# Kernel optimization log

Hardware: AMD Instinct MI355X
Metric: run time of the kernel (lower is better)

Reference implementation:

```python
import jax, jax.numpy as jnp
import numpy as np

N_EDGES = 1_600_000
D_FEAT = 32
N_NODES = 50_000


def setup_inputs() -> dict:
    key = jax.random.key(0)
    k1, k2, k3, k4 = jax.random.split(key, 4)
    m = jax.random.normal(k1, (N_EDGES, D_FEAT), dtype=jnp.float32)
    dst = jax.random.randint(k2, (N_EDGES,), 0, N_NODES, dtype=jnp.int64)
    w = jax.random.normal(k3, (4,), dtype=jnp.float32)
    b = jax.random.normal(k4, (1,), dtype=jnp.float32)
    return {"m": m, "dst": dst, "w": w, "b": b, "n_nodes": N_NODES}


def reference(m, dst, w, b, n_nodes):
    # Four segment reductions edge->node over destination index (copy_e_*)
    s = jax.ops.segment_sum(m, dst, num_segments=n_nodes)            # [N, D]
    mn = jax.ops.segment_min(m, dst, num_segments=n_nodes)
    mx = jax.ops.segment_max(m, dst, num_segments=n_nodes)
    deg = jax.ops.segment_sum(jnp.ones((m.shape[0],), m.dtype), dst,
                              num_segments=n_nodes)                  # [N]
    has = (deg > 0)[:, None]
    # DGL returns 0 for zero-degree nodes
    mn = jnp.where(has, mn, 0.0)
    mx = jnp.where(has, mx, 0.0)
    mean = s / jnp.maximum(deg, 1.0)[:, None]
    stacked = jnp.stack([s, mn, mx, mean], axis=-1)                  # [N, D, 4]
    out = jnp.einsum('ndk,k->nd', stacked, w) + b[0]                 # Dense(4,1) + squeeze
    return out
```

## Files before the change

kernel.cpp:

```cpp
#include <hip/hip_runtime.h>
#include <math.h>

#define D_FEAT 32
#define BSHIFT 5
#define NODES_PER_BKT 32
#define TILE 8192
#define PT 32
#define MAXBKT 2048
#define CAP 2048

__global__ void hist_kernel(const int* __restrict__ dst, int* __restrict__ bucketCount,
                            int E4, int nbucket) {
    __shared__ int h[MAXBKT];
    for (int i = threadIdx.x; i < nbucket; i += 256) h[i] = 0;
    __syncthreads();
    const int4* dst4 = (const int4*)dst;
    int tbase4 = blockIdx.x * (TILE / 4);
    #pragma unroll
    for (int k = 0; k < PT / 4; k++) {
        int i4 = tbase4 + k * 256 + threadIdx.x;
        if (i4 < E4) {
            int4 d = dst4[i4];
            atomicAdd(&h[d.x >> BSHIFT], 1);
            atomicAdd(&h[d.y >> BSHIFT], 1);
            atomicAdd(&h[d.z >> BSHIFT], 1);
            atomicAdd(&h[d.w >> BSHIFT], 1);
        }
    }
    __syncthreads();
    for (int i = threadIdx.x; i < nbucket; i += 256) {
        int c = h[i];
        if (c) atomicAdd(&bucketCount[i], c);
    }
}

__global__ void scan_kernel(const int* __restrict__ bucketCount,
                            int* __restrict__ bucketBase, int* __restrict__ bucketCursor,
                            int nbucket, int E) {
    __shared__ int lds[256];
    int tid = threadIdx.x;
    int vals[8];
    int s = 0;
    #pragma unroll
    for (int k = 0; k < 8; k++) {
        int i = tid * 8 + k;
        vals[k] = (i < nbucket) ? bucketCount[i] : 0;
        s += vals[k];
    }
    lds[tid] = s;
    __syncthreads();
    for (int off = 1; off < 256; off <<= 1) {
        int t = (tid >= off) ? lds[tid - off] : 0;
        __syncthreads();
        lds[tid] += t;
        __syncthreads();
    }
    int run = lds[tid] - s;
    #pragma unroll
    for (int k = 0; k < 8; k++) {
        int i = tid * 8 + k;
        if (i < nbucket) { bucketBase[i] = run; bucketCursor[i] = run; }
        run += vals[k];
    }
    if (tid == 0) bucketBase[nbucket] = E;
}

__global__ void partition_kernel(const int* __restrict__ dst,
                                 int* __restrict__ bucketCursor,
                                 unsigned int* __restrict__ keys,
                                 int E4, int nbucket) {
    __shared__ int h[MAXBKT];
    __shared__ int baseL[MAXBKT];
    int tid = threadIdx.x;
    for (int i = tid; i < nbucket; i += 256) h[i] = 0;
    __syncthreads();
    const int4* dst4 = (const int4*)dst;
    int tbase4 = blockIdx.x * (TILE / 4);
    int pk[PT];
    #pragma unroll
    for (int k = 0; k < PT / 4; k++) {
        int i4 = tbase4 + k * 256 + tid;
        if (i4 < E4) {
            int4 d = dst4[i4];
            int b0 = d.x >> BSHIFT; int r0 = atomicAdd(&h[b0], 1);
            int b1 = d.y >> BSHIFT; int r1 = atomicAdd(&h[b1], 1);
            int b2 = d.z >> BSHIFT; int r2 = atomicAdd(&h[b2], 1);
            int b3 = d.w >> BSHIFT; int r3 = atomicAdd(&h[b3], 1);
            pk[4 * k + 0] = (b0 << 18) | ((d.x & (NODES_PER_BKT - 1)) << 13) | r0;
            pk[4 * k + 1] = (b1 << 18) | ((d.y & (NODES_PER_BKT - 1)) << 13) | r1;
            pk[4 * k + 2] = (b2 << 18) | ((d.z & (NODES_PER_BKT - 1)) << 13) | r2;
            pk[4 * k + 3] = (b3 << 18) | ((d.w & (NODES_PER_BKT - 1)) << 13) | r3;
        } else {
            pk[4 * k + 0] = -1; pk[4 * k + 1] = -1;
            pk[4 * k + 2] = -1; pk[4 * k + 3] = -1;
        }
    }
    __syncthreads();
    for (int i = tid; i < nbucket; i += 256) {
        int c = h[i];
        baseL[i] = c ? atomicAdd(&bucketCursor[i], c) : 0;
    }
    __syncthreads();
    #pragma unroll
    for (int k = 0; k < PT / 4; k++) {
        int i4 = tbase4 + k * 256 + tid;
        int e = i4 * 4;
        #pragma unroll
        for (int l = 0; l < 4; l++) {
            int p = pk[4 * k + l];
            if (p >= 0) {
                int b   = p >> 18;
                int loc = (p >> 13) & (NODES_PER_BKT - 1);
                int r   = p & 8191;
                keys[baseL[b] + r] = ((unsigned)loc << 26) | (unsigned)(e + l);
            }
        }
    }
}

__global__ __launch_bounds__(256) void bucket_gather_kernel(
        const float* __restrict__ m,
        const unsigned int* __restrict__ keys,
        const int* __restrict__ bucketBase,
        const float* __restrict__ w,
        const float* __restrict__ bia,
        float* __restrict__ out, int N) {
    __shared__ unsigned int ukey[CAP];
    __shared__ int seid[CAP];
    __shared__ int nh[NODES_PER_BKT];
    __shared__ int noff[NODES_PER_BKT + 1];
    __shared__ int ncur[NODES_PER_BKT];
    int bkt = blockIdx.x;
    int tid = threadIdx.x;
    int start = bucketBase[bkt];
    int cnt = bucketBase[bkt + 1] - start;
    if (cnt > CAP) cnt = CAP;

    if (tid < NODES_PER_BKT) nh[tid] = 0;
    __syncthreads();
    for (int i = tid; i < cnt; i += 256) {
        unsigned int k = keys[start + i];
        ukey[i] = k;
        atomicAdd(&nh[k >> 26], 1);
    }
    __syncthreads();
    if (tid < NODES_PER_BKT) {
        int v = nh[tid];
        int x = v;
        #pragma unroll
        for (int off = 1; off < NODES_PER_BKT; off <<= 1) {
            int t = __shfl_up(x, off, 64);
            if (tid >= off) x += t;
        }
        noff[tid + 1] = x;
        if (tid == 0) noff[0] = 0;
        ncur[tid] = x - v;
    }
    __syncthreads();
    for (int i = tid; i < cnt; i += 256) {
        unsigned int k = ukey[i];
        int pos = atomicAdd(&ncur[k >> 26], 1);
        seid[pos] = (int)(k & 0x03FFFFFFu);
    }
    __syncthreads();

    const int fo  = tid & 7;
    const int grp = tid >> 3;
    const int node = (bkt << BSHIFT) + grp;
    const int s0 = noff[grp];
    const int e0 = noff[grp + 1];
    const int deg = e0 - s0;
    const float w0 = w[0], w1 = w[1], w2 = w[2], w3 = w[3], bb = bia[0];

    float sa0 = 0.f, sa1 = 0.f, sa2 = 0.f, sa3 = 0.f;
    float mn0 = INFINITY, mn1 = INFINITY, mn2 = INFINITY, mn3 = INFINITY;
    float mx0 = -INFINITY, mx1 = -INFINITY, mx2 = -INFINITY, mx3 = -INFINITY;

#define ACC(v)                                              \
    sa0 += (v).x; mn0 = fminf(mn0, (v).x); mx0 = fmaxf(mx0, (v).x); \
    sa1 += (v).y; mn1 = fminf(mn1, (v).y); mx1 = fmaxf(mx1, (v).y); \
    sa2 += (v).z; mn2 = fminf(mn2, (v).z); mx2 = fmaxf(mx2, (v).z); \
    sa3 += (v).w; mn3 = fminf(mn3, (v).w); mx3 = fmaxf(mx3, (v).w);

    int j = s0;
    for (; j + 4 <= e0; j += 4) {
        int ea = seid[j], eb = seid[j + 1], ec = seid[j + 2], ed = seid[j + 3];
        float4 va = *(const float4*)&m[ea * D_FEAT + (fo << 2)];
        float4 vb = *(const float4*)&m[eb * D_FEAT + (fo << 2)];
        float4 vc = *(const float4*)&m[ec * D_FEAT + (fo << 2)];
        float4 vd = *(const float4*)&m[ed * D_FEAT + (fo << 2)];
        ACC(va); ACC(vb); ACC(vc); ACC(vd);
    }
    for (; j < e0; j++) {
        float4 v = *(const float4*)&m[seid[j] * D_FEAT + (fo << 2)];
        ACC(v);
    }
#undef ACC

    if (node < N) {
        bool has = deg > 0;
        float inv = 1.0f / fmaxf((float)deg, 1.0f);
        float4 o;
        o.x = w0 * sa0 + w1 * (has ? mn0 : 0.f) + w2 * (has ? mx0 : 0.f) + w3 * (sa0 * inv) + bb;
        o.y = w0 * sa1 + w1 * (has ? mn1 : 0.f) + w2 * (has ? mx1 : 0.f) + w3 * (sa1 * inv) + bb;
        o.z = w0 * sa2 + w1 * (has ? mn2 : 0.f) + w2 * (has ? mx2 : 0.f) + w3 * (sa2 * inv) + bb;
        o.w = w0 * sa3 + w1 * (has ? mn3 : 0.f) + w2 * (has ? mx3 : 0.f) + w3 * (sa3 * inv) + bb;
        *(float4*)&out[node * D_FEAT + (fo << 2)] = o;
    }
}

extern "C" void kernel_launch(void* const* d_in, const int* in_sizes, int n_in,
                              void* d_out, int out_size, void* d_ws, size_t ws_size,
                              hipStream_t stream) {
    const float* m   = (const float*)d_in[0];
    const int*   dst = (const int*)  d_in[1];
    const float* w   = (const float*)d_in[2];
    const float* b   = (const float*)d_in[3];

    int E = in_sizes[0] / D_FEAT;
    int N = out_size    / D_FEAT;
    int E4 = E / 4;
    int nbucket = (N + NODES_PER_BKT - 1) >> BSHIFT;

    int* ws           = (int*)d_ws;
    int* bucketCount  = ws;
    int* bucketBase   = bucketCount + MAXBKT;
    int* bucketCursor = bucketBase + MAXBKT + 1;
    unsigned int* keys = (unsigned int*)(bucketCursor + MAXBKT);

    int nTiles = (E + TILE - 1) / TILE;

    hipMemsetAsync(bucketCount, 0, MAXBKT * sizeof(int), stream);
    hipLaunchKernelGGL(hist_kernel, dim3(nTiles), dim3(256), 0, stream,
                       dst, bucketCount, E4, nbucket);
    hipLaunchKernelGGL(scan_kernel, dim3(1), dim3(256), 0, stream,
                       bucketCount, bucketBase, bucketCursor, nbucket, E);
    hipLaunchKernelGGL(partition_kernel, dim3(nTiles), dim3(256), 0, stream,
                       dst, bucketCursor, keys, E4, nbucket);
    hipLaunchKernelGGL(bucket_gather_kernel, dim3(nbucket), dim3(256), 0, stream,
                       m, keys, bucketBase, w, b, (float*)d_out, N);
}
```

Measured before the change: 335.1 us.

## Widen buckets to 128 nodes and stage partitioned keys in LDS

Buckets grow from 32 to 128 nodes, so there are 391 buckets instead of 1563. The partition kernel now does a local scan and stages keys in shared memory sorted by bucket, then writes each bucket's run to global memory, instead of scattering keys directly. The gather kernel uses 512 threads that loop over two node groups, with a larger seid buffer and no ukey copy, re-reading keys from global memory. The goal is fewer global atomics on the bucket cursors and more contiguous key writes, at the cost of a large LDS footprint (32 KB stage buffer) and a copy loop where each thread serially writes one bucket's run.

```diff
diff --git a/kernel.cpp b/kernel.cpp
--- a/kernel.cpp
+++ b/kernel.cpp
@@ -2,17 +2,19 @@
 #include <math.h>
 
 #define D_FEAT 32
-#define BSHIFT 5
-#define NODES_PER_BKT 32
+#define BSHIFT 7
+#define NODES_PER_BKT 128
 #define TILE 8192
 #define PT 32
-#define MAXBKT 2048
-#define CAP 2048
-
-__global__ void hist_kernel(const int* __restrict__ dst, int* __restrict__ bucketCount,
-                            int E4, int nbucket) {
+#define MAXBKT 512
+#define CAPG 5120
+#define GBLK 512
+
+__global__ __launch_bounds__(256) void hist_kernel(const int* __restrict__ dst,
+                                                   int* __restrict__ bucketCount,
+                                                   int E4, int nbucket) {
     __shared__ int h[MAXBKT];
-    for (int i = threadIdx.x; i < nbucket; i += 256) h[i] = 0;
+    for (int i = threadIdx.x; i < MAXBKT; i += 256) h[i] = 0;
     __syncthreads();
     const int4* dst4 = (const int4*)dst;
     int tbase4 = blockIdx.x * (TILE / 4);
@@ -34,19 +36,15 @@
     }
 }
 
-__global__ void scan_kernel(const int* __restrict__ bucketCount,
-                            int* __restrict__ bucketBase, int* __restrict__ bucketCursor,
-                            int nbucket, int E) {
+__global__ __launch_bounds__(256) void scan_kernel(const int* __restrict__ bucketCount,
+                                                   int* __restrict__ bucketBase,
+                                                   int* __restrict__ bucketCursor,
+                                                   int nbucket, int E) {
     __shared__ int lds[256];
     int tid = threadIdx.x;
-    int vals[8];
-    int s = 0;
-    #pragma unroll
-    for (int k = 0; k < 8; k++) {
-        int i = tid * 8 + k;
-        vals[k] = (i < nbucket) ? bucketCount[i] : 0;
-        s += vals[k];
-    }
+    int v0 = bucketCount[2 * tid];
+    int v1 = bucketCount[2 * tid + 1];
+    int s = v0 + v1;
     lds[tid] = s;
     __syncthreads();
     for (int off = 1; off < 256; off <<= 1) {
@@ -56,77 +54,91 @@
         __syncthreads();
     }
     int run = lds[tid] - s;
-    #pragma unroll
-    for (int k = 0; k < 8; k++) {
-        int i = tid * 8 + k;
-        if (i < nbucket) { bucketBase[i] = run; bucketCursor[i] = run; }
-        run += vals[k];
-    }
-    if (tid == 0) bucketBase[nbucket] = E;
-}
-
-__global__ void partition_kernel(const int* __restrict__ dst,
-                                 int* __restrict__ bucketCursor,
-                                 unsigned int* __restrict__ keys,
-                                 int E4, int nbucket) {
+    bucketBase[2 * tid] = run;       bucketCursor[2 * tid] = run;
+    bucketBase[2 * tid + 1] = run + v0; bucketCursor[2 * tid + 1] = run + v0;
+    if (tid == 255) bucketBase[512] = run + s;
+}
+
+__global__ __launch_bounds__(256) void partition_kernel(const int* __restrict__ dst,
+                                                        int* __restrict__ bucketCursor,
+                                                        unsigned int* __restrict__ keys,
+                                                        int E4, int nbucket) {
     __shared__ int h[MAXBKT];
-    __shared__ int baseL[MAXBKT];
+    __shared__ int hoff[MAXBKT + 1];
+    __shared__ int gbase[MAXBKT];
+    __shared__ int scanb[256];
+    __shared__ unsigned int stage[TILE];
     int tid = threadIdx.x;
-    for (int i = tid; i < nbucket; i += 256) h[i] = 0;
+    for (int i = tid; i < MAXBKT; i += 256) h[i] = 0;
     __syncthreads();
     const int4* dst4 = (const int4*)dst;
     int tbase4 = blockIdx.x * (TILE / 4);
-    int pk[PT];
     #pragma unroll
     for (int k = 0; k < PT / 4; k++) {
         int i4 = tbase4 + k * 256 + tid;
         if (i4 < E4) {
             int4 d = dst4[i4];
-            int b0 = d.x >> BSHIFT; int r0 = atomicAdd(&h[b0], 1);
-            int b1 = d.y >> BSHIFT; int r1 = atomicAdd(&h[b1], 1);
-            int b2 = d.z >> BSHIFT; int r2 = atomicAdd(&h[b2], 1);
-            int b3 = d.w >> BSHIFT; int r3 = atomicAdd(&h[b3], 1);
-            pk[4 * k + 0] = (b0 << 18) | ((d.x & (NODES_PER_BKT - 1)) << 13) | r0;
-            pk[4 * k + 1] = (b1 << 18) | ((d.y & (NODES_PER_BKT - 1)) << 13) | r1;
-            pk[4 * k + 2] = (b2 << 18) | ((d.z & (NODES_PER_BKT - 1)) << 13) | r2;
-            pk[4 * k + 3] = (b3 << 18) | ((d.w & (NODES_PER_BKT - 1)) << 13) | r3;
-        } else {
-            pk[4 * k + 0] = -1; pk[4 * k + 1] = -1;
-            pk[4 * k + 2] = -1; pk[4 * k + 3] = -1;
-        }
-    }
-    __syncthreads();
+            atomicAdd(&h[d.x >> BSHIFT], 1);
+            atomicAdd(&h[d.y >> BSHIFT], 1);
+            atomicAdd(&h[d.z >> BSHIFT], 1);
+            atomicAdd(&h[d.w >> BSHIFT], 1);
+        }
+    }
+    __syncthreads();
+    int v0 = h[2 * tid], v1 = h[2 * tid + 1];
+    int s = v0 + v1;
+    scanb[tid] = s;
+    __syncthreads();
+    for (int off = 1; off < 256; off <<= 1) {
+        int t = (tid >= off) ? scanb[tid - off] : 0;
+        __syncthreads();
+        scanb[tid] += t;
+        __syncthreads();
+    }
+    int run = scanb[tid] - s;
+    hoff[2 * tid] = run;
+    hoff[2 * tid + 1] = run + v0;
+    if (tid == 255) hoff[512] = run + s;
     for (int i = tid; i < nbucket; i += 256) {
         int c = h[i];
-        baseL[i] = c ? atomicAdd(&bucketCursor[i], c) : 0;
-    }
+        gbase[i] = c ? atomicAdd(&bucketCursor[i], c) : 0;
+    }
+    __syncthreads();
+    for (int i = tid; i < MAXBKT; i += 256) h[i] = hoff[i];
     __syncthreads();
     #pragma unroll
     for (int k = 0; k < PT / 4; k++) {
         int i4 = tbase4 + k * 256 + tid;
-        int e = i4 * 4;
-        #pragma unroll
-        for (int l = 0; l < 4; l++) {
-            int p = pk[4 * k + l];
-            if (p >= 0) {
-                int b   = p >> 18;
-                int loc = (p >> 13) & (NODES_PER_BKT - 1);
-                int r   = p & 8191;
-                keys[baseL[b] + r] = ((unsigned)loc << 26) | (unsigned)(e + l);
-            }
-        }
-    }
-}
-
-__global__ __launch_bounds__(256) void bucket_gather_kernel(
+        if (i4 < E4) {
+            int4 d = dst4[i4];
+            int e = i4 * 4;
+            int r;
+            r = atomicAdd(&h[d.x >> BSHIFT], 1);
+            stage[r] = ((unsigned)(d.x & (NODES_PER_BKT - 1)) << 21) | (unsigned)e;
+            r = atomicAdd(&h[d.y >> BSHIFT], 1);
+            stage[r] = ((unsigned)(d.y & (NODES_PER_BKT - 1)) << 21) | (unsigned)(e + 1);
+            r = atomicAdd(&h[d.z >> BSHIFT], 1);
+            stage[r] = ((unsigned)(d.z & (NODES_PER_BKT - 1)) << 21) | (unsigned)(e + 2);
+            r = atomicAdd(&h[d.w >> BSHIFT], 1);
+            stage[r] = ((unsigned)(d.w & (NODES_PER_BKT - 1)) << 21) | (unsigned)(e + 3);
+        }
+    }
+    __syncthreads();
+    for (int i = tid; i < nbucket; i += 256) {
+        int lo = hoff[i], hi = hoff[i + 1];
+        int g = gbase[i];
+        for (int j = lo; j < hi; j++) keys[g + (j - lo)] = stage[j];
+    }
+}
+
+__global__ __launch_bounds__(GBLK) void bucket_gather_kernel(
         const float* __restrict__ m,
         const unsigned int* __restrict__ keys,
         const int* __restrict__ bucketBase,
         const float* __restrict__ w,
         const float* __restrict__ bia,
         float* __restrict__ out, int N) {
-    __shared__ unsigned int ukey[CAP];
-    __shared__ int seid[CAP];
+    __shared__ int seid[CAPG];
     __shared__ int nh[NODES_PER_BKT];
     __shared__ int noff[NODES_PER_BKT + 1];
     __shared__ int ncur[NODES_PER_BKT];
@@ -134,70 +146,70 @@
     int tid = threadIdx.x;
     int start = bucketBase[bkt];
     int cnt = bucketBase[bkt + 1] - start;
-    if (cnt > CAP) cnt = CAP;
-
-    if (tid < NODES_PER_BKT) nh[tid] = 0;
-    __syncthreads();
-    for (int i = tid; i < cnt; i += 256) {
-        unsigned int k = keys[start + i];
-        ukey[i] = k;
-        atomicAdd(&nh[k >> 26], 1);
-    }
-    __syncthreads();
-    if (tid < NODES_PER_BKT) {
-        int v = nh[tid];
-        int x = v;
+    if (cnt > CAPG) cnt = CAPG;
+
+    for (int i = tid; i < NODES_PER_BKT; i += GBLK) nh[i] = 0;
+    __syncthreads();
+    for (int i = tid; i < cnt; i += GBLK)
+        atomicAdd(&nh[keys[start + i] >> 21], 1);
+    __syncthreads();
+    if (tid < 64) {
+        int a0 = nh[2 * tid], a1 = nh[2 * tid + 1];
+        int s = a0 + a1;
+        int x = s;
         #pragma unroll
-        for (int off = 1; off < NODES_PER_BKT; off <<= 1) {
+        for (int off = 1; off < 64; off <<= 1) {
             int t = __shfl_up(x, off, 64);
             if (tid >= off) x += t;
         }
-        noff[tid + 1] = x;
-        if (tid == 0) noff[0] = 0;
-        ncur[tid] = x - v;
-    }
-    __syncthreads();
-    for (int i = tid; i < cnt; i += 256) {
-        unsigned int k = ukey[i];
-        int pos = atomicAdd(&ncur[k >> 26], 1);
-        seid[pos] = (int)(k & 0x03FFFFFFu);
+        int base = x - s;
+        noff[2 * tid] = base;      ncur[2 * tid] = base;
+        noff[2 * tid + 1] = base + a0; ncur[2 * tid + 1] = base + a0;
+        if (tid == 63) noff[NODES_PER_BKT] = x;
+    }
+    __syncthreads();
+    for (int i = tid; i < cnt; i += GBLK) {
+        unsigned int k = keys[start + i];
+        int pos = atomicAdd(&ncur[k >> 21], 1);
+        seid[pos] = (int)(k & 0x1FFFFFu);
     }
     __syncthreads();
 
     const int fo  = tid & 7;
     const int grp = tid >> 3;
-    const int node = (bkt << BSHIFT) + grp;
-    const int s0 = noff[grp];
-    const int e0 = noff[grp + 1];
-    const int deg = e0 - s0;
     const float w0 = w[0], w1 = w[1], w2 = w[2], w3 = w[3], bb = bia[0];
 
-    float sa0 = 0.f, sa1 = 0.f, sa2 = 0.f, sa3 = 0.f;
-    float mn0 = INFINITY, mn1 = INFINITY, mn2 = INFINITY, mn3 = INFINITY;
-    float mx0 = -INFINITY, mx1 = -INFINITY, mx2 = -INFINITY, mx3 = -INFINITY;
-
-#define ACC(v)                                              \
-    sa0 += (v).x; mn0 = fminf(mn0, (v).x); mx0 = fmaxf(mx0, (v).x); \
-    sa1 += (v).y; mn1 = fminf(mn1, (v).y); mx1 = fmaxf(mx1, (v).y); \
-    sa2 += (v).z; mn2 = fminf(mn2, (v).z); mx2 = fmaxf(mx2, (v).z); \
-    sa3 += (v).w; mn3 = fminf(mn3, (v).w); mx3 = fmaxf(mx3, (v).w);
-
-    int j = s0;
-    for (; j + 4 <= e0; j += 4) {
-        int ea = seid[j], eb = seid[j + 1], ec = seid[j + 2], ed = seid[j + 3];
-        float4 va = *(const float4*)&m[ea * D_FEAT + (fo << 2)];
-        float4 vb = *(const float4*)&m[eb * D_FEAT + (fo << 2)];
-        float4 vc = *(const float4*)&m[ec * D_FEAT + (fo << 2)];
-        float4 vd = *(const float4*)&m[ed * D_FEAT + (fo << 2)];
-        ACC(va); ACC(vb); ACC(vc); ACC(vd);
-    }
-    for (; j < e0; j++) {
-        float4 v = *(const float4*)&m[seid[j] * D_FEAT + (fo << 2)];
-        ACC(v);
-    }
+    for (int nl = grp; nl < NODES_PER_BKT; nl += 64) {
+        int node = (bkt << BSHIFT) + nl;
+        if (node >= N) break;
+        int s0 = noff[nl];     if (s0 > cnt) s0 = cnt;
+        int e0 = noff[nl + 1]; if (e0 > cnt) e0 = cnt;
+        int deg = e0 - s0;
+        float sa0 = 0.f, sa1 = 0.f, sa2 = 0.f, sa3 = 0.f;
+        float mn0 = INFINITY, mn1 = INFINITY, mn2 = INFINITY, mn3 = INFINITY;
+        float mx0 = -INFINITY, mx1 = -INFINITY, mx2 = -INFINITY, mx3 = -INFINITY;
+
+#define ACC(v)                                                      \
+        sa0 += (v).x; mn0 = fminf(mn0, (v).x); mx0 = fmaxf(mx0, (v).x); \
+        sa1 += (v).y; mn1 = fminf(mn1, (v).y); mx1 = fmaxf(mx1, (v).y); \
+        sa2 += (v).z; mn2 = fminf(mn2, (v).z); mx2 = fmaxf(mx2, (v).z); \
+        sa3 += (v).w; mn3 = fminf(mn3, (v).w); mx3 = fmaxf(mx3, (v).w);
+
+        int j = s0;
+        for (; j + 4 <= e0; j += 4) {
+            int ea = seid[j], eb = seid[j + 1], ec = seid[j + 2], ed = seid[j + 3];
+            float4 va = *(const float4*)&m[ea * D_FEAT + (fo << 2)];
+            float4 vb = *(const float4*)&m[eb * D_FEAT + (fo << 2)];
+            float4 vc = *(const float4*)&m[ec * D_FEAT + (fo << 2)];
+            float4 vd = *(const float4*)&m[ed * D_FEAT + (fo << 2)];
+            ACC(va); ACC(vb); ACC(vc); ACC(vd);
+        }
+        for (; j < e0; j++) {
+            float4 v = *(const float4*)&m[seid[j] * D_FEAT + (fo << 2)];
+            ACC(v);
+        }
 #undef ACC
 
-    if (node < N) {
         bool has = deg > 0;
         float inv = 1.0f / fmaxf((float)deg, 1.0f);
         float4 o;
@@ -237,6 +249,6 @@
                        bucketCount, bucketBase, bucketCursor, nbucket, E);
     hipLaunchKernelGGL(partition_kernel, dim3(nTiles), dim3(256), 0, stream,
                        dst, bucketCursor, keys, E4, nbucket);
-    hipLaunchKernelGGL(bucket_gather_kernel, dim3(nbucket), dim3(256), 0, stream,
+    hipLaunchKernelGGL(bucket_gather_kernel, dim3(nbucket), dim3(GBLK), 0, stream,
                        m, keys, bucketBase, w, b, (float*)d_out, N);
 }
```

After: 329.2 us. About the same (-1.8%).

## Fuse histogram, scan, partition and gather into one cooperative kernel

Applied to the files above, without the earlier changes.

Replaces the memset and four separate kernel launches with a single cooperative persistent kernel of 1024 blocks. The phases are separated by grid-wide syncs, and a shared-memory union lets each phase reuse the same LDS. This removes launch gaps and the memset, but adds four grid barriers and caps the gather phase at a fixed grid that loops over buckets. Occupancy may also drop because every block reserves the largest union member (16 KB).

```diff
diff --git a/kernel.cpp b/kernel.cpp
--- a/kernel.cpp
+++ b/kernel.cpp
@@ -1,211 +1,230 @@
 #include <hip/hip_runtime.h>
+#include <hip/hip_cooperative_groups.h>
 #include <math.h>
+
+namespace cg = cooperative_groups;
 
 #define D_FEAT 32
 #define BSHIFT 5
-#define NODES_PER_BKT 32
+#define NPB 32
 #define TILE 8192
 #define PT 32
 #define MAXBKT 2048
 #define CAP 2048
-
-__global__ void hist_kernel(const int* __restrict__ dst, int* __restrict__ bucketCount,
-                            int E4, int nbucket) {
-    __shared__ int h[MAXBKT];
-    for (int i = threadIdx.x; i < nbucket; i += 256) h[i] = 0;
-    __syncthreads();
-    const int4* dst4 = (const int4*)dst;
-    int tbase4 = blockIdx.x * (TILE / 4);
-    #pragma unroll
-    for (int k = 0; k < PT / 4; k++) {
-        int i4 = tbase4 + k * 256 + threadIdx.x;
-        if (i4 < E4) {
-            int4 d = dst4[i4];
-            atomicAdd(&h[d.x >> BSHIFT], 1);
-            atomicAdd(&h[d.y >> BSHIFT], 1);
-            atomicAdd(&h[d.z >> BSHIFT], 1);
-            atomicAdd(&h[d.w >> BSHIFT], 1);
-        }
-    }
-    __syncthreads();
-    for (int i = threadIdx.x; i < nbucket; i += 256) {
-        int c = h[i];
-        if (c) atomicAdd(&bucketCount[i], c);
-    }
-}
-
-__global__ void scan_kernel(const int* __restrict__ bucketCount,
-                            int* __restrict__ bucketBase, int* __restrict__ bucketCursor,
-                            int nbucket, int E) {
-    __shared__ int lds[256];
-    int tid = threadIdx.x;
-    int vals[8];
-    int s = 0;
-    #pragma unroll
-    for (int k = 0; k < 8; k++) {
-        int i = tid * 8 + k;
-        vals[k] = (i < nbucket) ? bucketCount[i] : 0;
-        s += vals[k];
-    }
-    lds[tid] = s;
-    __syncthreads();
-    for (int off = 1; off < 256; off <<= 1) {
-        int t = (tid >= off) ? lds[tid - off] : 0;
-        __syncthreads();
-        lds[tid] += t;
-        __syncthreads();
-    }
-    int run = lds[tid] - s;
-    #pragma unroll
-    for (int k = 0; k < 8; k++) {
-        int i = tid * 8 + k;
-        if (i < nbucket) { bucketBase[i] = run; bucketCursor[i] = run; }
-        run += vals[k];
-    }
-    if (tid == 0) bucketBase[nbucket] = E;
-}
-
-__global__ void partition_kernel(const int* __restrict__ dst,
-                                 int* __restrict__ bucketCursor,
-                                 unsigned int* __restrict__ keys,
-                                 int E4, int nbucket) {
-    __shared__ int h[MAXBKT];
-    __shared__ int baseL[MAXBKT];
-    int tid = threadIdx.x;
-    for (int i = tid; i < nbucket; i += 256) h[i] = 0;
-    __syncthreads();
-    const int4* dst4 = (const int4*)dst;
-    int tbase4 = blockIdx.x * (TILE / 4);
-    int pk[PT];
-    #pragma unroll
-    for (int k = 0; k < PT / 4; k++) {
-        int i4 = tbase4 + k * 256 + tid;
-        if (i4 < E4) {
-            int4 d = dst4[i4];
-            int b0 = d.x >> BSHIFT; int r0 = atomicAdd(&h[b0], 1);
-            int b1 = d.y >> BSHIFT; int r1 = atomicAdd(&h[b1], 1);
-            int b2 = d.z >> BSHIFT; int r2 = atomicAdd(&h[b2], 1);
-            int b3 = d.w >> BSHIFT; int r3 = atomicAdd(&h[b3], 1);
-            pk[4 * k + 0] = (b0 << 18) | ((d.x & (NODES_PER_BKT - 1)) << 13) | r0;
-            pk[4 * k + 1] = (b1 << 18) | ((d.y & (NODES_PER_BKT - 1)) << 13) | r1;
-            pk[4 * k + 2] = (b2 << 18) | ((d.z & (NODES_PER_BKT - 1)) << 13) | r2;
-            pk[4 * k + 3] = (b3 << 18) | ((d.w & (NODES_PER_BKT - 1)) << 13) | r3;
-        } else {
-            pk[4 * k + 0] = -1; pk[4 * k + 1] = -1;
-            pk[4 * k + 2] = -1; pk[4 * k + 3] = -1;
-        }
-    }
-    __syncthreads();
-    for (int i = tid; i < nbucket; i += 256) {
-        int c = h[i];
-        baseL[i] = c ? atomicAdd(&bucketCursor[i], c) : 0;
-    }
-    __syncthreads();
-    #pragma unroll
-    for (int k = 0; k < PT / 4; k++) {
-        int i4 = tbase4 + k * 256 + tid;
-        int e = i4 * 4;
-        #pragma unroll
-        for (int l = 0; l < 4; l++) {
-            int p = pk[4 * k + l];
-            if (p >= 0) {
-                int b   = p >> 18;
-                int loc = (p >> 13) & (NODES_PER_BKT - 1);
-                int r   = p & 8191;
-                keys[baseL[b] + r] = ((unsigned)loc << 26) | (unsigned)(e + l);
-            }
-        }
-    }
-}
-
-__global__ __launch_bounds__(256) void bucket_gather_kernel(
+#define GRID 1024
+#define BLK 256
+
+union SmemU {
+    int hist[MAXBKT];
+    int scan[BLK];
+    struct { int h[MAXBKT]; int baseL[MAXBKT]; } p;
+    struct {
+        unsigned int ukey[CAP];
+        int seid[CAP];
+        int nh[NPB];
+        int noff[NPB + 1];
+        int ncur[NPB];
+    } g;
+};
+
+__global__ __launch_bounds__(BLK, 4) void fused_kernel(
         const float* __restrict__ m,
-        const unsigned int* __restrict__ keys,
-        const int* __restrict__ bucketBase,
+        const int* __restrict__ dst,
         const float* __restrict__ w,
         const float* __restrict__ bia,
-        float* __restrict__ out, int N) {
-    __shared__ unsigned int ukey[CAP];
-    __shared__ int seid[CAP];
-    __shared__ int nh[NODES_PER_BKT];
-    __shared__ int noff[NODES_PER_BKT + 1];
-    __shared__ int ncur[NODES_PER_BKT];
-    int bkt = blockIdx.x;
-    int tid = threadIdx.x;
-    int start = bucketBase[bkt];
-    int cnt = bucketBase[bkt + 1] - start;
-    if (cnt > CAP) cnt = CAP;
-
-    if (tid < NODES_PER_BKT) nh[tid] = 0;
-    __syncthreads();
-    for (int i = tid; i < cnt; i += 256) {
-        unsigned int k = keys[start + i];
-        ukey[i] = k;
-        atomicAdd(&nh[k >> 26], 1);
-    }
-    __syncthreads();
-    if (tid < NODES_PER_BKT) {
-        int v = nh[tid];
-        int x = v;
-        #pragma unroll
-        for (int off = 1; off < NODES_PER_BKT; off <<= 1) {
-            int t = __shfl_up(x, off, 64);
-            if (tid >= off) x += t;
-        }
-        noff[tid + 1] = x;
-        if (tid == 0) noff[0] = 0;
-        ncur[tid] = x - v;
-    }
-    __syncthreads();
-    for (int i = tid; i < cnt; i += 256) {
-        unsigned int k = ukey[i];
-        int pos = atomicAdd(&ncur[k >> 26], 1);
-        seid[pos] = (int)(k & 0x03FFFFFFu);
-    }
-    __syncthreads();
-
+        float* __restrict__ out,
+        int* __restrict__ bucketCount,
+        int* __restrict__ bucketBase,
+        int* __restrict__ bucketCursor,
+        unsigned int* __restrict__ keys,
+        int E, int N, int nbucket, int nTiles) {
+    cg::grid_group grid = cg::this_grid();
+    __shared__ SmemU S;
+    const int tid = threadIdx.x;
+    const int bid = blockIdx.x;
+    const int E4 = E >> 2;
+    const int4* dst4 = (const int4*)dst;
+
+    for (int i = bid * BLK + tid; i < MAXBKT; i += GRID * BLK) bucketCount[i] = 0;
+    grid.sync();
+
+    if (bid < nTiles) {
+        for (int i = tid; i < MAXBKT; i += BLK) S.hist[i] = 0;
+        __syncthreads();
+        int tbase4 = bid * (TILE / 4);
+        #pragma unroll
+        for (int k = 0; k < PT / 4; k++) {
+            int i4 = tbase4 + k * BLK + tid;
+            if (i4 < E4) {
+                int4 d = dst4[i4];
+                atomicAdd(&S.hist[d.x >> BSHIFT], 1);
+                atomicAdd(&S.hist[d.y >> BSHIFT], 1);
+                atomicAdd(&S.hist[d.z >> BSHIFT], 1);
+                atomicAdd(&S.hist[d.w >> BSHIFT], 1);
+            }
+        }
+        __syncthreads();
+        for (int i = tid; i < nbucket; i += BLK) {
+            int c = S.hist[i];
+            if (c) atomicAdd(&bucketCount[i], c);
+        }
+    }
+    grid.sync();
+
+    if (bid == 0) {
+        int vals[8];
+        int s = 0;
+        #pragma unroll
+        for (int k = 0; k < 8; k++) {
+            int i = tid * 8 + k;
+            vals[k] = (i < nbucket) ? bucketCount[i] : 0;
+            s += vals[k];
+        }
+        S.scan[tid] = s;
+        __syncthreads();
+        for (int off = 1; off < BLK; off <<= 1) {
+            int t = (tid >= off) ? S.scan[tid - off] : 0;
+            __syncthreads();
+            S.scan[tid] += t;
+            __syncthreads();
+        }
+        int run = S.scan[tid] - s;
+        #pragma unroll
+        for (int k = 0; k < 8; k++) {
+            int i = tid * 8 + k;
+            if (i < nbucket) { bucketBase[i] = run; bucketCursor[i] = run; }
+            run += vals[k];
+        }
+        if (tid == 0) bucketBase[nbucket] = E;
+    }
+    grid.sync();
+
+    if (bid < nTiles) {
+        for (int i = tid; i < MAXBKT; i += BLK) S.p.h[i] = 0;
+        __syncthreads();
+        int tbase4 = bid * (TILE / 4);
+        int pk[PT];
+        #pragma unroll
+        for (int k = 0; k < PT / 4; k++) {
+            int i4 = tbase4 + k * BLK + tid;
+            if (i4 < E4) {
+                int4 d = dst4[i4];
+                int b0 = d.x >> BSHIFT; int r0 = atomicAdd(&S.p.h[b0], 1);
+                int b1 = d.y >> BSHIFT; int r1 = atomicAdd(&S.p.h[b1], 1);
+                int b2 = d.z >> BSHIFT; int r2 = atomicAdd(&S.p.h[b2], 1);
+                int b3 = d.w >> BSHIFT; int r3 = atomicAdd(&S.p.h[b3], 1);
+                pk[4 * k + 0] = (b0 << 18) | ((d.x & (NPB - 1)) << 13) | r0;
+                pk[4 * k + 1] = (b1 << 18) | ((d.y & (NPB - 1)) << 13) | r1;
+                pk[4 * k + 2] = (b2 << 18) | ((d.z & (NPB - 1)) << 13) | r2;
+                pk[4 * k + 3] = (b3 << 18) | ((d.w & (NPB - 1)) << 13) | r3;
+            } else {
+                pk[4 * k + 0] = -1; pk[4 * k + 1] = -1;
+                pk[4 * k + 2] = -1; pk[4 * k + 3] = -1;
+            }
+        }
+        __syncthreads();
+        for (int i = tid; i < nbucket; i += BLK) {
+            int c = S.p.h[i];
+            S.p.baseL[i] = c ? atomicAdd(&bucketCursor[i], c) : 0;
+        }
+        __syncthreads();
+        #pragma unroll
+        for (int k = 0; k < PT / 4; k++) {
+            int i4 = tbase4 + k * BLK + tid;
+            int e = i4 * 4;
+            #pragma unroll
+            for (int l = 0; l < 4; l++) {
+                int p = pk[4 * k + l];
+                if (p >= 0) {
+                    int b   = p >> 18;
+                    int loc = (p >> 13) & (NPB - 1);
+                    int r   = p & 8191;
+                    keys[S.p.baseL[b] + r] = ((unsigned)loc << 26) | (unsigned)(e + l);
+                }
+            }
+        }
+    }
+    grid.sync();
+
+    const float w0 = w[0], w1 = w[1], w2 = w[2], w3 = w[3], bb = bia[0];
     const int fo  = tid & 7;
     const int grp = tid >> 3;
-    const int node = (bkt << BSHIFT) + grp;
-    const int s0 = noff[grp];
-    const int e0 = noff[grp + 1];
-    const int deg = e0 - s0;
-    const float w0 = w[0], w1 = w[1], w2 = w[2], w3 = w[3], bb = bia[0];
-
-    float sa0 = 0.f, sa1 = 0.f, sa2 = 0.f, sa3 = 0.f;
-    float mn0 = INFINITY, mn1 = INFINITY, mn2 = INFINITY, mn3 = INFINITY;
-    float mx0 = -INFINITY, mx1 = -INFINITY, mx2 = -INFINITY, mx3 = -INFINITY;
+
+    for (int bkt = bid; bkt < nbucket; bkt += GRID) {
+        __syncthreads();
+        int start = bucketBase[bkt];
+        int cnt = bucketBase[bkt + 1] - start;
+        if (cnt > CAP) cnt = CAP;
+
+        if (tid < NPB) S.g.nh[tid] = 0;
+        __syncthreads();
+        for (int i = tid; i < cnt; i += BLK) {
+            unsigned int k = keys[start + i];
+            S.g.ukey[i] = k;
+            atomicAdd(&S.g.nh[k >> 26], 1);
+        }
+        __syncthreads();
+        if (tid < NPB) {
+            int v = S.g.nh[tid];
+            int x = v;
+            #pragma unroll
+            for (int off = 1; off < NPB; off <<= 1) {
+                int t = __shfl_up(x, off, 64);
+                if (tid >= off) x += t;
+            }
+            S.g.noff[tid + 1] = x;
+            if (tid == 0) S.g.noff[0] = 0;
+            S.g.ncur[tid] = x - v;
+        }
+        __syncthreads();
+        for (int i = tid; i < cnt; i += BLK) {
+            unsigned int k = S.g.ukey[i];
+            int pos = atomicAdd(&S.g.ncur[k >> 26], 1);
+            S.g.seid[pos] = (int)(k & 0x03FFFFFFu);
+        }
+        __syncthreads();
+
+        const int node = (bkt << BSHIFT) + grp;
+        const int s0 = S.g.noff[grp];
+        const int e0 = S.g.noff[grp + 1];
+        const int deg = e0 - s0;
+
+        float sa0 = 0.f, sa1 = 0.f, sa2 = 0.f, sa3 = 0.f;
+        float mn0 = INFINITY, mn1 = INFINITY, mn2 = INFINITY, mn3 = INFINITY;
+        float mx0 = -INFINITY, mx1 = -INFINITY, mx2 = -INFINITY, mx3 = -INFINITY;
 
 #define ACC(v)                                              \
-    sa0 += (v).x; mn0 = fminf(mn0, (v).x); mx0 = fmaxf(mx0, (v).x); \
-    sa1 += (v).y; mn1 = fminf(mn1, (v).y); mx1 = fmaxf(mx1, (v).y); \
-    sa2 += (v).z; mn2 = fminf(mn2, (v).z); mx2 = fmaxf(mx2, (v).z); \
-    sa3 += (v).w; mn3 = fminf(mn3, (v).w); mx3 = fmaxf(mx3, (v).w);
-
-    int j = s0;
-    for (; j + 4 <= e0; j += 4) {
-        int ea = seid[j], eb = seid[j + 1], ec = seid[j + 2], ed = seid[j + 3];
-        float4 va = *(const float4*)&m[ea * D_FEAT + (fo << 2)];
-        float4 vb = *(const float4*)&m[eb * D_FEAT + (fo << 2)];
-        float4 vc = *(const float4*)&m[ec * D_FEAT + (fo << 2)];
-        float4 vd = *(const float4*)&m[ed * D_FEAT + (fo << 2)];
-        ACC(va); ACC(vb); ACC(vc); ACC(vd);
-    }
-    for (; j < e0; j++) {
-        float4 v = *(const float4*)&m[seid[j] * D_FEAT + (fo << 2)];
-        ACC(v);
-    }
+        sa0 += (v).x; mn0 = fminf(mn0, (v).x); mx0 = fmaxf(mx0, (v).x); \
+        sa1 += (v).y; mn1 = fminf(mn1, (v).y); mx1 = fmaxf(mx1, (v).y); \
+        sa2 += (v).z; mn2 = fminf(mn2, (v).z); mx2 = fmaxf(mx2, (v).z); \
+        sa3 += (v).w; mn3 = fminf(mn3, (v).w); mx3 = fmaxf(mx3, (v).w);
+
+        int j = s0;
+        for (; j + 4 <= e0; j += 4) {
+            int ea = S.g.seid[j], eb = S.g.seid[j + 1];
+            int ec = S.g.seid[j + 2], ed = S.g.seid[j + 3];
+            float4 va = *(const float4*)&m[ea * D_FEAT + (fo << 2)];
+            float4 vb = *(const float4*)&m[eb * D_FEAT + (fo << 2)];
+            float4 vc = *(const float4*)&m[ec * D_FEAT + (fo << 2)];
+            float4 vd = *(const float4*)&m[ed * D_FEAT + (fo << 2)];
+            ACC(va); ACC(vb); ACC(vc); ACC(vd);
+        }
+        for (; j < e0; j++) {
+            float4 v = *(const float4*)&m[S.g.seid[j] * D_FEAT + (fo << 2)];
+            ACC(v);
+        }
 #undef ACC
 
-    if (node < N) {
-        bool has = deg > 0;
-        float inv = 1.0f / fmaxf((float)deg, 1.0f);
-        float4 o;
-        o.x = w0 * sa0 + w1 * (has ? mn0 : 0.f) + w2 * (has ? mx0 : 0.f) + w3 * (sa0 * inv) + bb;
-        o.y = w0 * sa1 + w1 * (has ? mn1 : 0.f) + w2 * (has ? mx1 : 0.f) + w3 * (sa1 * inv) + bb;
-        o.z = w0 * sa2 + w1 * (has ? mn2 : 0.f) + w2 * (has ? mx2 : 0.f) + w3 * (sa2 * inv) + bb;
-        o.w = w0 * sa3 + w1 * (has ? mn3 : 0.f) + w2 * (has ? mx3 : 0.f) + w3 * (sa3 * inv) + bb;
-        *(float4*)&out[node * D_FEAT + (fo << 2)] = o;
+        if (node < N) {
+            bool has = deg > 0;
+            float inv = 1.0f / fmaxf((float)deg, 1.0f);
+            float4 o;
+            o.x = w0 * sa0 + w1 * (has ? mn0 : 0.f) + w2 * (has ? mx0 : 0.f) + w3 * (sa0 * inv) + bb;
+            o.y = w0 * sa1 + w1 * (has ? mn1 : 0.f) + w2 * (has ? mx1 : 0.f) + w3 * (sa1 * inv) + bb;
+            o.z = w0 * sa2 + w1 * (has ? mn2 : 0.f) + w2 * (has ? mx2 : 0.f) + w3 * (sa2 * inv) + bb;
+            o.w = w0 * sa3 + w1 * (has ? mn3 : 0.f) + w2 * (has ? mx3 : 0.f) + w3 * (sa3 * inv) + bb;
+            *(float4*)&out[node * D_FEAT + (fo << 2)] = o;
+        }
     }
 }
 
@@ -216,11 +235,12 @@
     const int*   dst = (const int*)  d_in[1];
     const float* w   = (const float*)d_in[2];
     const float* b   = (const float*)d_in[3];
+    float* outp = (float*)d_out;
 
     int E = in_sizes[0] / D_FEAT;
     int N = out_size    / D_FEAT;
-    int E4 = E / 4;
-    int nbucket = (N + NODES_PER_BKT - 1) >> BSHIFT;
+    int nbucket = (N + NPB - 1) >> BSHIFT;
+    int nTiles = (E + TILE - 1) / TILE;
 
     int* ws           = (int*)d_ws;
     int* bucketCount  = ws;
@@ -228,15 +248,11 @@
     int* bucketCursor = bucketBase + MAXBKT + 1;
     unsigned int* keys = (unsigned int*)(bucketCursor + MAXBKT);
 
-    int nTiles = (E + TILE - 1) / TILE;
-
-    hipMemsetAsync(bucketCount, 0, MAXBKT * sizeof(int), stream);
-    hipLaunchKernelGGL(hist_kernel, dim3(nTiles), dim3(256), 0, stream,
-                       dst, bucketCount, E4, nbucket);
-    hipLaunchKernelGGL(scan_kernel, dim3(1), dim3(256), 0, stream,
-                       bucketCount, bucketBase, bucketCursor, nbucket, E);
-    hipLaunchKernelGGL(partition_kernel, dim3(nTiles), dim3(256), 0, stream,
-                       dst, bucketCursor, keys, E4, nbucket);
-    hipLaunchKernelGGL(bucket_gather_kernel, dim3(nbucket), dim3(256), 0, stream,
-                       m, keys, bucketBase, w, b, (float*)d_out, N);
+    void* args[] = {
+        (void*)&m, (void*)&dst, (void*)&w, (void*)&b, (void*)&outp,
+        (void*)&bucketCount, (void*)&bucketBase, (void*)&bucketCursor,
+        (void*)&keys, (void*)&E, (void*)&N, (void*)&nbucket, (void*)&nTiles
+    };
+    hipLaunchCooperativeKernel((void*)fused_kernel, dim3(GRID), dim3(BLK),
+                               args, 0, stream);
 }
```

After: 697.2 us. 108% more time.
